# Performance work log

Measured on AMD Instinct MI355X. Metric: run time of the kernel, lower is better.

Reference implementation:

```python
import jax, jax.numpy as jnp
import numpy as np

K = 7          # local attention kernel size
PAD = 3        # (K-1)//2 so output spatial dims match input
GROUPS = 8

def unfold2d(x, k):
    # x: [B, C, H+k-1, W+k-1] -> patches [B, C, H, W, k*k] (kh-major, kw-minor, matching F.unfold)
    B, C, Hp, Wp = x.shape
    H, W = Hp - k + 1, Wp - k + 1
    return jnp.stack([x[:, :, i:i + H, j:j + W] for i in range(k) for j in range(k)], axis=-1)

def setup_inputs():
    key = jax.random.key(0)
    k1, k2, k3, k4, k5, k6 = jax.random.split(key, 6)
    B, Cin, H, W = 2, 256, 56, 56
    outc = 256
    scale = (2.0 / Cin) ** 0.5  # kaiming fan_out-ish init
    return {
        "feature_map": jax.random.normal(k1, (B, 2 * Cin, H, W), jnp.float32),
        "w_q": jax.random.normal(k2, (outc, Cin), jnp.float32) * scale,
        "w_k": jax.random.normal(k3, (outc, Cin), jnp.float32) * scale,
        "w_v": jax.random.normal(k4, (outc, Cin), jnp.float32) * scale,
        "rel_h": jax.random.normal(k5, (outc // 2, K), jnp.float32),
        "rel_w": jax.random.normal(k6, (outc // 2, K), jnp.float32),
    }

def reference(feature_map, w_q, w_k, w_v, rel_h, rel_w):
    B, C2, H, W = feature_map.shape
    Cin = C2 // 2
    fm_t0, fm_t1 = feature_map[:, :Cin], feature_map[:, Cin:]
    outc = w_q.shape[0]
    # 1x1 convs (bias=False)
    q = jnp.einsum('oc,bchw->bohw', w_q, fm_t1)                      # [B, outc, H, W]
    padded = jnp.pad(fm_t0, ((0, 0), (0, 0), (PAD, PAD), (PAD, PAD)))
    kk = jnp.einsum('oc,bchw->bohw', w_k, padded)
    vv = jnp.einsum('oc,bchw->bohw', w_v, padded)
    k_out = unfold2d(kk, K)                                          # [B, outc, H, W, K*K]
    v_out = unfold2d(vv, K)
    # relative position bias: first half channels get row bias, second half col bias
    half = outc // 2
    bias_h = jnp.broadcast_to(rel_h[:, :, None], (half, K, K)).reshape(half, K * K)
    bias_w = jnp.broadcast_to(rel_w[:, None, :], (half, K, K)).reshape(half, K * K)
    bias = jnp.concatenate([bias_h, bias_w], axis=0)                 # [outc, K*K]
    k_out = k_out + bias[None, :, None, None, :]
    G, Cg = GROUPS, outc // GROUPS
    qg = q.reshape(B, G, Cg, H, W)
    kg = k_out.reshape(B, G, Cg, H, W, K * K)
    vg = v_out.reshape(B, G, Cg, H, W, K * K)
    logits = jnp.einsum('bgchw,bgchwk->bghwk', qg, kg)
    wts = jax.nn.softmax(logits, axis=-1)
    out = jnp.einsum('bghwk,bgchwk->bgchw', wts, vg)
    return out.reshape(B, outc, H, W)
```

## Files before the change

### kernel.cpp

```cpp
#include <hip/hip_runtime.h>
#include <hip/hip_bf16.h>

#define B    2
#define CIN  256
#define H    56
#define W    56
#define OUTC 256
#define KS   7
#define PAD  3
#define G    8
#define CG   32
#define HP   62
#define WP   62
#define P1   (H * W)
#define P2   (HP * WP)

typedef __attribute__((ext_vector_type(2))) _Float16 h2;
typedef __attribute__((ext_vector_type(8))) _Float16 f16x8;
typedef __attribute__((ext_vector_type(8))) unsigned short ushort8;
typedef __attribute__((ext_vector_type(4))) float f32x4;

__device__ inline unsigned short f2h(float f) {
    const _Float16 h = (_Float16)f;
    return *(const unsigned short*)&h;
}

__device__ inline float fdot2(h2 a, h2 b, float c) {
#if defined(__has_builtin)
#if __has_builtin(__builtin_amdgcn_fdot2)
    return __builtin_amdgcn_fdot2(a, b, c, false);
#else
    return c + (float)a[0] * (float)b[0] + (float)a[1] * (float)b[1];
#endif
#else
    return c + (float)a[0] * (float)b[0] + (float)a[1] * (float)b[1];
#endif
}

__device__ inline float dot8(const f16x8 q, const f16x8 k, float s) {
    s = fdot2((h2){q[0], q[1]}, (h2){k[0], k[1]}, s);
    s = fdot2((h2){q[2], q[3]}, (h2){k[2], k[3]}, s);
    s = fdot2((h2){q[4], q[5]}, (h2){k[4], k[5]}, s);
    s = fdot2((h2){q[6], q[7]}, (h2){k[6], k[7]}, s);
    return s;
}

#define ASTR 40
__global__ __launch_bounds__(256, 2) void gemm_kernel(const float* __restrict__ fm,
                                                      const float* __restrict__ wq,
                                                      const float* __restrict__ wk,
                                                      const float* __restrict__ wv,
                                                      unsigned short* __restrict__ qi,
                                                      unsigned short* __restrict__ ki,
                                                      unsigned short* __restrict__ vi) {
    const int b = blockIdx.z;
    const bool isQ = blockIdx.y < 2;
    if (isQ && blockIdx.x >= 25) return;
    const int o0 = (isQ ? blockIdx.y : (blockIdx.y - 2)) * 128;
    const int n0 = blockIdx.x * 128;
    const int Nreal = isQ ? P1 : P2;
    const int Pstr  = isQ ? P1 : P2;

    const float* Wsrc;
    int orow0;
    if (isQ)            { Wsrc = wq; orow0 = o0; }
    else if (o0 < 256)  { Wsrc = wk; orow0 = o0; }
    else                { Wsrc = wv; orow0 = o0 - 256; }

    __shared__ unsigned short Alds[128 * ASTR];
    __shared__ unsigned short Blds[128 * ASTR];
    const int tid = threadIdx.x;
    const int lane = tid & 63;
    const int wave = tid >> 6;
    const int wr = (wave >> 1) * 64;
    const int wc = (wave & 1) * 64;
    const int lrow = lane & 15;
    const int quad = lane >> 4;

    const int arow = tid & 127;
    const int akc  = (tid >> 7) * 16;

    const int n = n0 + arow;
    int srcoff = -1;
    if (isQ) {
        if (n < P1) srcoff = n;
    } else {
        if (n < P2) {
            const int y = n / WP, x = n - y * WP;
            const int iy = y - PAD, ix = x - PAD;
            if (iy >= 0 && iy < H && ix >= 0 && ix < W) srcoff = iy * W + ix;
        }
    }
    const float* fmB = fm + ((size_t)b * (2 * CIN) + (isQ ? CIN : 0)) * P1;
    const float* wrow = Wsrc + (size_t)orow0 * CIN + (size_t)arow * CIN + akc;

    unsigned short* alp = Alds + arow * ASTR + akc;
    unsigned short* blp = Blds + arow * ASTR + akc;

    f32x4 acc[4][4] = {};

    float av[16], bv[16];
    {
        const float4 a0 = ((const float4*)wrow)[0];
        const float4 a1 = ((const float4*)wrow)[1];
        const float4 a2 = ((const float4*)wrow)[2];
        const float4 a3 = ((const float4*)wrow)[3];
        av[0]=a0.x; av[1]=a0.y; av[2]=a0.z; av[3]=a0.w;
        av[4]=a1.x; av[5]=a1.y; av[6]=a1.z; av[7]=a1.w;
        av[8]=a2.x; av[9]=a2.y; av[10]=a2.z; av[11]=a2.w;
        av[12]=a3.x; av[13]=a3.y; av[14]=a3.z; av[15]=a3.w;
        #pragma unroll
        for (int j = 0; j < 16; ++j)
            bv[j] = (srcoff >= 0) ? fmB[(size_t)(akc + j) * P1 + srcoff] : 0.f;
    }

    for (int kb = 0; kb < CIN / 32; ++kb) {
        {
            f16x8 p0, p1, p2, p3;
            #pragma unroll
            for (int j = 0; j < 8; ++j) {
                p0[j] = (_Float16)av[j];
                p1[j] = (_Float16)av[8 + j];
                p2[j] = (_Float16)bv[j];
                p3[j] = (_Float16)bv[8 + j];
            }
            *(f16x8*)(alp)     = p0;
            *(f16x8*)(alp + 8) = p1;
            *(f16x8*)(blp)     = p2;
            *(f16x8*)(blp + 8) = p3;
        }
        __syncthreads();
        if (kb < CIN / 32 - 1) {
            const int c0 = (kb + 1) * 32 + akc;
            const float* wnext = wrow + (kb + 1) * 32;
            const float4 a0 = ((const float4*)wnext)[0];
            const float4 a1 = ((const float4*)wnext)[1];
            const float4 a2 = ((const float4*)wnext)[2];
            const float4 a3 = ((const float4*)wnext)[3];
            av[0]=a0.x; av[1]=a0.y; av[2]=a0.z; av[3]=a0.w;
            av[4]=a1.x; av[5]=a1.y; av[6]=a1.z; av[7]=a1.w;
            av[8]=a2.x; av[9]=a2.y; av[10]=a2.z; av[11]=a2.w;
            av[12]=a3.x; av[13]=a3.y; av[14]=a3.z; av[15]=a3.w;
            #pragma unroll
            for (int j = 0; j < 16; ++j)
                bv[j] = (srcoff >= 0) ? fmB[(size_t)(c0 + j) * P1 + srcoff] : 0.f;
        }
        f16x8 af[4], bfr[4];
        #pragma unroll
        for (int mi = 0; mi < 4; ++mi)
            af[mi] = *(const f16x8*)&Alds[(wr + mi * 16 + lrow) * ASTR + quad * 8];
        #pragma unroll
        for (int ni = 0; ni < 4; ++ni)
            bfr[ni] = *(const f16x8*)&Blds[(wc + ni * 16 + lrow) * ASTR + quad * 8];
        #pragma unroll
        for (int mi = 0; mi < 4; ++mi)
            #pragma unroll
            for (int ni = 0; ni < 4; ++ni)
                acc[mi][ni] = __builtin_amdgcn_mfma_f32_16x16x32_f16(af[mi], bfr[ni], acc[mi][ni], 0, 0, 0);
        __syncthreads();
    }

    #pragma unroll
    for (int mi = 0; mi < 4; ++mi) {
        const int gmBase = o0 + wr + mi * 16 + quad * 4;
        int ch0;
        unsigned short* base;
        if (isQ)               { ch0 = gmBase;       base = qi; }
        else if (gmBase < 256) { ch0 = gmBase;       base = ki; }
        else                   { ch0 = gmBase - 256; base = vi; }
        const int g   = ch0 >> 5;
        const int sub = (ch0 >> 3) & 3;
        const int l8  = ch0 & 7;
        unsigned short* pbase = base + ((((size_t)b * 8 + g) * 4 + sub) * Pstr) * 8 + l8;
        #pragma unroll
        for (int ni = 0; ni < 4; ++ni) {
            const int gn = n0 + wc + ni * 16 + lrow;
            if (gn < Nreal) {
                ushort4 pk;
                pk.x = f2h(acc[mi][ni][0]);
                pk.y = f2h(acc[mi][ni][1]);
                pk.z = f2h(acc[mi][ni][2]);
                pk.w = f2h(acc[mi][ni][3]);
                *(ushort4*)(pbase + (size_t)gn * 8) = pk;
            }
        }
    }
}

#define NPOS4 620
#define HALFE 1240
__global__ __launch_bounds__(128) void attn_kernel(const unsigned short* __restrict__ qi,
                                                   const unsigned short* __restrict__ ki,
                                                   const unsigned short* __restrict__ vi,
                                                   const float* __restrict__ rel_h,
                                                   const float* __restrict__ rel_w,
                                                   float* __restrict__ out) {
    __shared__ f16x8 sbuf[2 * HALFE];

    const int b  = blockIdx.z;
    const int g  = blockIdx.y;
    const int r0 = blockIdx.x * 4;
    const int oc0 = g * CG;
    const int tid = threadIdx.x;
    const bool active = tid < 112;
    const int rp = tid / 56;
    const int cx = tid - rp * 56;
    const int pr0 = r0 + 2 * rp;
    const int pix0 = pr0 * W + cx;
    const int pix1 = pix0 + W;

    const size_t bg4 = ((size_t)b * 8 + g) * 4;
    const size_t rowoff8 = ((size_t)r0 * WP) * 8;

    f16x8* bufA = sbuf;
    f16x8* bufB = sbuf + HALFE;

    f16x8 qh0[4], qh1[4];
    if (active) {
        #pragma unroll
        for (int sub = 0; sub < 4; ++sub) {
            qh0[sub] = *(const f16x8*)(qi + ((bg4 + sub) * P1 + pix0) * 8);
            qh1[sub] = *(const f16x8*)(qi + ((bg4 + sub) * P1 + pix1) * 8);
        }
    }

    f16x8 st[10];
    {
        const unsigned short* gb = ki + bg4 * P2 * 8 + rowoff8;
        #pragma unroll
        for (int it = 0; it < 10; ++it) {
            const int e = tid + it * 128;
            if (e < HALFE) {
                const int sl = (e >= NPOS4);
                const int pos = e - (sl ? NPOS4 : 0);
                st[it] = *(const f16x8*)(gb + ((size_t)sl * P2 + pos) * 8);
            }
        }
        #pragma unroll
        for (int it = 0; it < 10; ++it) {
            const int e = tid + it * 128;
            if (e < HALFE) bufA[e] = st[it];
        }
    }
    __syncthreads();

    {
        const unsigned short* gb = ki + (bg4 + 2) * P2 * 8 + rowoff8;
        #pragma unroll
        for (int it = 0; it < 10; ++it) {
            const int e = tid + it * 128;
            if (e < HALFE) {
                const int sl = (e >= NPOS4);
                const int pos = e - (sl ? NPOS4 : 0);
                st[it] = *(const f16x8*)(gb + ((size_t)sl * P2 + pos) * 8);
            }
        }
    }

    float logits0[KS * KS], logits1[KS * KS];
    if (active) {
        const float* rel = (g < 4) ? (rel_h + oc0 * KS) : (rel_w + (oc0 - 128) * KS);
        float qf0[32], qf1[32];
        #pragma unroll
        for (int sub = 0; sub < 4; ++sub)
            #pragma unroll
            for (int j = 0; j < 8; ++j) {
                qf0[sub * 8 + j] = (float)qh0[sub][j];
                qf1[sub * 8 + j] = (float)qh1[sub][j];
            }
        float bd0[KS], bd1[KS];
        #pragma unroll
        for (int t = 0; t < KS; ++t) {
            float s0 = 0.f, s1 = 0.f;
            #pragma unroll
            for (int c = 0; c < 32; ++c) {
                const float r = rel[c * KS + t];
                s0 += qf0[c] * r;
                s1 += qf1[c] * r;
            }
            bd0[t] = s0; bd1[t] = s1;
        }
        #pragma unroll
        for (int i = 0; i < KS; ++i)
            #pragma unroll
            for (int j = 0; j < KS; ++j) {
                logits0[i * KS + j] = (g < 4) ? bd0[i] : bd0[j];
                logits1[i * KS + j] = (g < 4) ? bd1[i] : bd1[j];
            }

        #pragma unroll
        for (int s = 0; s < 2; ++s) {
            const f16x8 q0 = qh0[s];
            const f16x8 q1 = qh1[s];
            #pragma unroll
            for (int j = 0; j < KS; ++j) {
                #pragma unroll
                for (int ii = 0; ii < 8; ++ii) {
                    const f16x8 kv = bufA[s * NPOS4 + (2 * rp + ii) * WP + cx + j];
                    if (ii < 7)  logits0[ii * KS + j]       = dot8(q0, kv, logits0[ii * KS + j]);
                    if (ii >= 1) logits1[(ii - 1) * KS + j] = dot8(q1, kv, logits1[(ii - 1) * KS + j]);
                }
            }
        }
    }
    #pragma unroll
    for (int it = 0; it < 10; ++it) {
        const int e = tid + it * 128;
        if (e < HALFE) bufB[e] = st[it];
    }
    __syncthreads();

    {
        const unsigned short* gb = vi + bg4 * P2 * 8 + rowoff8;
        #pragma unroll
        for (int it = 0; it < 10; ++it) {
            const int e = tid + it * 128;
            if (e < HALFE) {
                const int sl = (e >= NPOS4);
                const int pos = e - (sl ? NPOS4 : 0);
                st[it] = *(const f16x8*)(gb + ((size_t)sl * P2 + pos) * 8);
            }
        }
    }

    if (active) {
        #pragma unroll
        for (int s = 0; s < 2; ++s) {
            const f16x8 q0 = qh0[2 + s];
            const f16x8 q1 = qh1[2 + s];
            #pragma unroll
            for (int j = 0; j < KS; ++j) {
                #pragma unroll
                for (int ii = 0; ii < 8; ++ii) {
                    const f16x8 kv = bufB[s * NPOS4 + (2 * rp + ii) * WP + cx + j];
                    if (ii < 7)  logits0[ii * KS + j]       = dot8(q0, kv, logits0[ii * KS + j]);
                    if (ii >= 1) logits1[(ii - 1) * KS + j] = dot8(q1, kv, logits1[(ii - 1) * KS + j]);
                }
            }
        }
        {
            float m = logits0[0];
            #pragma unroll
            for (int t = 1; t < KS * KS; ++t) m = fmaxf(m, logits0[t]);
            float sum = 0.f;
            #pragma unroll
            for (int t = 0; t < KS * KS; ++t) {
                const float e = __expf(logits0[t] - m);
                logits0[t] = e;
                sum += e;
            }
            const float inv = 1.f / sum;
            #pragma unroll
            for (int t = 0; t < KS * KS; ++t) logits0[t] *= inv;
        }
        {
            float m = logits1[0];
            #pragma unroll
            for (int t = 1; t < KS * KS; ++t) m = fmaxf(m, logits1[t]);
            float sum = 0.f;
            #pragma unroll
            for (int t = 0; t < KS * KS; ++t) {
                const float e = __expf(logits1[t] - m);
                logits1[t] = e;
                sum += e;
            }
            const float inv = 1.f / sum;
            #pragma unroll
            for (int t = 0; t < KS * KS; ++t) logits1[t] *= inv;
        }
    }
    #pragma unroll
    for (int it = 0; it < 10; ++it) {
        const int e = tid + it * 128;
        if (e < HALFE) bufA[e] = st[it];
    }
    __syncthreads();

    {
        const unsigned short* gb = vi + (bg4 + 2) * P2 * 8 + rowoff8;
        #pragma unroll
        for (int it = 0; it < 10; ++it) {
            const int e = tid + it * 128;
            if (e < HALFE) {
                const int sl = (e >= NPOS4);
                const int pos = e - (sl ? NPOS4 : 0);
                st[it] = *(const f16x8*)(gb + ((size_t)sl * P2 + pos) * 8);
            }
        }
    }

    if (active) {
        #pragma unroll
        for (int s = 0; s < 2; ++s) {
            float a0[8] = {}, a1[8] = {};
            #pragma unroll
            for (int j = 0; j < KS; ++j) {
                #pragma unroll
                for (int ii = 0; ii < 8; ++ii) {
                    const f16x8 v = bufA[s * NPOS4 + (2 * rp + ii) * WP + cx + j];
                    if (ii < 7) {
                        const float wt = logits0[ii * KS + j];
                        #pragma unroll
                        for (int c = 0; c < 8; ++c) a0[c] += wt * (float)v[c];
                    }
                    if (ii >= 1) {
                        const float wt = logits1[(ii - 1) * KS + j];
                        #pragma unroll
                        for (int c = 0; c < 8; ++c) a1[c] += wt * (float)v[c];
                    }
                }
            }
            float* op0 = out + ((size_t)b * OUTC + oc0 + s * 8) * P1 + pix0;
            float* op1 = out + ((size_t)b * OUTC + oc0 + s * 8) * P1 + pix1;
            #pragma unroll
            for (int c = 0; c < 8; ++c) {
                op0[(size_t)c * P1] = a0[c];
                op1[(size_t)c * P1] = a1[c];
            }
        }
    }
    #pragma unroll
    for (int it = 0; it < 10; ++it) {
        const int e = tid + it * 128;
        if (e < HALFE) bufB[e] = st[it];
    }
    __syncthreads();

    if (active) {
        #pragma unroll
        for (int s = 0; s < 2; ++s) {
            float a0[8] = {}, a1[8] = {};
            #pragma unroll
            for (int j = 0; j < KS; ++j) {
                #pragma unroll
                for (int ii = 0; ii < 8; ++ii) {
                    const f16x8 v = bufB[s * NPOS4 + (2 * rp + ii) * WP + cx + j];
                    if (ii < 7) {
                        const float wt = logits0[ii * KS + j];
                        #pragma unroll
                        for (int c = 0; c < 8; ++c) a0[c] += wt * (float)v[c];
                    }
                    if (ii >= 1) {
                        const float wt = logits1[(ii - 1) * KS + j];
                        #pragma unroll
                        for (int c = 0; c < 8; ++c) a1[c] += wt * (float)v[c];
                    }
                }
            }
            float* op0 = out + ((size_t)b * OUTC + oc0 + 16 + s * 8) * P1 + pix0;
            float* op1 = out + ((size_t)b * OUTC + oc0 + 16 + s * 8) * P1 + pix1;
            #pragma unroll
            for (int c = 0; c < 8; ++c) {
                op0[(size_t)c * P1] = a0[c];
                op1[(size_t)c * P1] = a1[c];
            }
        }
    }
}

extern "C" void kernel_launch(void* const* d_in, const int* in_sizes, int n_in,
                              void* d_out, int out_size, void* d_ws, size_t ws_size,
                              hipStream_t stream) {
    const float* fm = (const float*)d_in[0];
    const float* wq = (const float*)d_in[1];
    const float* wk = (const float*)d_in[2];
    const float* wv = (const float*)d_in[3];
    const float* rh = (const float*)d_in[4];
    const float* rw = (const float*)d_in[5];
    float* out = (float*)d_out;

    unsigned short* ws = (unsigned short*)d_ws;
    unsigned short* qi = ws;
    unsigned short* ki = qi + (size_t)B * OUTC * P1;
    unsigned short* vi = ki + (size_t)B * OUTC * P2;

    gemm_kernel<<<dim3(31, 6, B), 256, 0, stream>>>(fm, wq, wk, wv, qi, ki, vi);
    attn_kernel<<<dim3(H / 4, G, B), 128, 0, stream>>>(qi, ki, vi, rh, rw, out);
}
```

Baseline: 108.6 us.

## Replace LDS-staged attention with one-pixel-per-thread direct global loads

```diff
diff --git a/kernel.cpp b/kernel.cpp
--- a/kernel.cpp
+++ b/kernel.cpp
@@ -187,273 +187,103 @@
     }
 }
 
-#define NPOS4 620
-#define HALFE 1240
-__global__ __launch_bounds__(128) void attn_kernel(const unsigned short* __restrict__ qi,
+__global__ __launch_bounds__(256) void attn_kernel(const unsigned short* __restrict__ qi,
                                                    const unsigned short* __restrict__ ki,
                                                    const unsigned short* __restrict__ vi,
                                                    const float* __restrict__ rel_h,
                                                    const float* __restrict__ rel_w,
                                                    float* __restrict__ out) {
-    __shared__ f16x8 sbuf[2 * HALFE];
-
-    const int b  = blockIdx.z;
-    const int g  = blockIdx.y;
-    const int r0 = blockIdx.x * 4;
-    const int oc0 = g * CG;
+    const int b = blockIdx.z;
+    const int g = blockIdx.y;
     const int tid = threadIdx.x;
-    const bool active = tid < 112;
-    const int rp = tid / 56;
-    const int cx = tid - rp * 56;
-    const int pr0 = r0 + 2 * rp;
-    const int pix0 = pr0 * W + cx;
-    const int pix1 = pix0 + W;
-
-    const size_t bg4 = ((size_t)b * 8 + g) * 4;
-    const size_t rowoff8 = ((size_t)r0 * WP) * 8;
-
-    f16x8* bufA = sbuf;
-    f16x8* bufB = sbuf + HALFE;
-
-    f16x8 qh0[4], qh1[4];
-    if (active) {
-        #pragma unroll
-        for (int sub = 0; sub < 4; ++sub) {
-            qh0[sub] = *(const f16x8*)(qi + ((bg4 + sub) * P1 + pix0) * 8);
-            qh1[sub] = *(const f16x8*)(qi + ((bg4 + sub) * P1 + pix1) * 8);
-        }
-    }
-
-    f16x8 st[10];
+
+    int p = blockIdx.x * 256 + tid;
+    const bool act = p < P1;
+    if (!act) p = P1 - 1;
+
+    const int h = p / W;
+    const int w = p - h * W;
+    const int pos0 = h * WP + w;
+    const size_t bg4 = ((size_t)b * G + g) * 4;
+
+    f16x8 qh[4];
+    #pragma unroll
+    for (int s = 0; s < 4; ++s)
+        qh[s] = *(const f16x8*)(qi + ((bg4 + s) * P1 + p) * 8);
+
+    const float* rel = (g < 4) ? (rel_h + (size_t)g * CG * KS)
+                               : (rel_w + (size_t)(g - 4) * CG * KS);
+    float bd[KS];
+    #pragma unroll
+    for (int t = 0; t < KS; ++t) {
+        float s0 = 0.f;
+        #pragma unroll
+        for (int s = 0; s < 4; ++s)
+            #pragma unroll
+            for (int j = 0; j < 8; ++j)
+                s0 += (float)qh[s][j] * rel[(s * 8 + j) * KS + t];
+        bd[t] = s0;
+    }
+
+    float logits[KS * KS];
+    #pragma unroll
+    for (int i = 0; i < KS; ++i)
+        #pragma unroll
+        for (int j = 0; j < KS; ++j)
+            logits[i * KS + j] = (g < 4) ? bd[i] : bd[j];
+
+    #pragma unroll
+    for (int s = 0; s < 4; ++s) {
+        const unsigned short* kp = ki + ((bg4 + s) * P2 + pos0) * 8;
+        const f16x8 q = qh[s];
+        #pragma unroll
+        for (int i = 0; i < KS; ++i) {
+            const unsigned short* kr = kp + i * WP * 8;
+            #pragma unroll
+            for (int j = 0; j < KS; ++j) {
+                const f16x8 kv = *(const f16x8*)(kr + j * 8);
+                logits[i * KS + j] = dot8(q, kv, logits[i * KS + j]);
+            }
+        }
+    }
+
     {
-        const unsigned short* gb = ki + bg4 * P2 * 8 + rowoff8;
-        #pragma unroll
-        for (int it = 0; it < 10; ++it) {
-            const int e = tid + it * 128;
-            if (e < HALFE) {
-                const int sl = (e >= NPOS4);
-                const int pos = e - (sl ? NPOS4 : 0);
-                st[it] = *(const f16x8*)(gb + ((size_t)sl * P2 + pos) * 8);
+        float m = logits[0];
+        #pragma unroll
+        for (int t = 1; t < KS * KS; ++t) m = fmaxf(m, logits[t]);
+        float sum = 0.f;
+        #pragma unroll
+        for (int t = 0; t < KS * KS; ++t) {
+            const float e = __expf(logits[t] - m);
+            logits[t] = e;
+            sum += e;
+        }
+        const float inv = 1.f / sum;
+        #pragma unroll
+        for (int t = 0; t < KS * KS; ++t) logits[t] *= inv;
+    }
+
+    #pragma unroll
+    for (int s = 0; s < 4; ++s) {
+        const unsigned short* vp = vi + ((bg4 + s) * P2 + pos0) * 8;
+        float a[8] = {};
+        #pragma unroll
+        for (int i = 0; i < KS; ++i) {
+            const unsigned short* vr = vp + i * WP * 8;
+            #pragma unroll
+            for (int j = 0; j < KS; ++j) {
+                const f16x8 vv = *(const f16x8*)(vr + j * 8);
+                const float wt = logits[i * KS + j];
+                #pragma unroll
+                for (int c = 0; c < 8; ++c)
+                    a[c] += wt * (float)vv[c];
             }
         }
-        #pragma unroll
-        for (int it = 0; it < 10; ++it) {
-            const int e = tid + it * 128;
-            if (e < HALFE) bufA[e] = st[it];
-        }
-    }
-    __syncthreads();
-
-    {
-        const unsigned short* gb = ki + (bg4 + 2) * P2 * 8 + rowoff8;
-        #pragma unroll
-        for (int it = 0; it < 10; ++it) {
-            const int e = tid + it * 128;
-            if (e < HALFE) {
-                const int sl = (e >= NPOS4);
-                const int pos = e - (sl ? NPOS4 : 0);
-                st[it] = *(const f16x8*)(gb + ((size_t)sl * P2 + pos) * 8);
-            }
-        }
-    }
-
-    float logits0[KS * KS], logits1[KS * KS];
-    if (active) {
-        const float* rel = (g < 4) ? (rel_h + oc0 * KS) : (rel_w + (oc0 - 128) * KS);
-        float qf0[32], qf1[32];
-        #pragma unroll
-        for (int sub = 0; sub < 4; ++sub)
-            #pragma unroll
-            for (int j = 0; j < 8; ++j) {
-                qf0[sub * 8 + j] = (float)qh0[sub][j];
-                qf1[sub * 8 + j] = (float)qh1[sub][j];
-            }
-        float bd0[KS], bd1[KS];
-        #pragma unroll
-        for (int t = 0; t < KS; ++t) {
-            float s0 = 0.f, s1 = 0.f;
-            #pragma unroll
-            for (int c = 0; c < 32; ++c) {
-                const float r = rel[c * KS + t];
-                s0 += qf0[c] * r;
-                s1 += qf1[c] * r;
-            }
-            bd0[t] = s0; bd1[t] = s1;
-        }
-        #pragma unroll
-        for (int i = 0; i < KS; ++i)
-            #pragma unroll
-            for (int j = 0; j < KS; ++j) {
-                logits0[i * KS + j] = (g < 4) ? bd0[i] : bd0[j];
-                logits1[i * KS + j] = (g < 4) ? bd1[i] : bd1[j];
-            }
-
-        #pragma unroll
-        for (int s = 0; s < 2; ++s) {
-            const f16x8 q0 = qh0[s];
-            const f16x8 q1 = qh1[s];
-            #pragma unroll
-            for (int j = 0; j < KS; ++j) {
-                #pragma unroll
-                for (int ii = 0; ii < 8; ++ii) {
-                    const f16x8 kv = bufA[s * NPOS4 + (2 * rp + ii) * WP + cx + j];
-                    if (ii < 7)  logits0[ii * KS + j]       = dot8(q0, kv, logits0[ii * KS + j]);
-                    if (ii >= 1) logits1[(ii - 1) * KS + j] = dot8(q1, kv, logits1[(ii - 1) * KS + j]);
-                }
-            }
-        }
-    }
-    #pragma unroll
-    for (int it = 0; it < 10; ++it) {
-        const int e = tid + it * 128;
-        if (e < HALFE) bufB[e] = st[it];
-    }
-    __syncthreads();
-
-    {
-        const unsigned short* gb = vi + bg4 * P2 * 8 + rowoff8;
-        #pragma unroll
-        for (int it = 0; it < 10; ++it) {
-            const int e = tid + it * 128;
-            if (e < HALFE) {
-                const int sl = (e >= NPOS4);
-                const int pos = e - (sl ? NPOS4 : 0);
-                st[it] = *(const f16x8*)(gb + ((size_t)sl * P2 + pos) * 8);
-            }
-        }
-    }
-
-    if (active) {
-        #pragma unroll
-        for (int s = 0; s < 2; ++s) {
-            const f16x8 q0 = qh0[2 + s];
-            const f16x8 q1 = qh1[2 + s];
-            #pragma unroll
-            for (int j = 0; j < KS; ++j) {
-                #pragma unroll
-                for (int ii = 0; ii < 8; ++ii) {
-                    const f16x8 kv = bufB[s * NPOS4 + (2 * rp + ii) * WP + cx + j];
-                    if (ii < 7)  logits0[ii * KS + j]       = dot8(q0, kv, logits0[ii * KS + j]);
-                    if (ii >= 1) logits1[(ii - 1) * KS + j] = dot8(q1, kv, logits1[(ii - 1) * KS + j]);
-                }
-            }
-        }
-        {
-            float m = logits0[0];
-            #pragma unroll
-            for (int t = 1; t < KS * KS; ++t) m = fmaxf(m, logits0[t]);
-            float sum = 0.f;
-            #pragma unroll
-            for (int t = 0; t < KS * KS; ++t) {
-                const float e = __expf(logits0[t] - m);
-                logits0[t] = e;
-                sum += e;
-            }
-            const float inv = 1.f / sum;
-            #pragma unroll
-            for (int t = 0; t < KS * KS; ++t) logits0[t] *= inv;
-        }
-        {
-            float m = logits1[0];
-            #pragma unroll
-            for (int t = 1; t < KS * KS; ++t) m = fmaxf(m, logits1[t]);
-            float sum = 0.f;
-            #pragma unroll
-            for (int t = 0; t < KS * KS; ++t) {
-                const float e = __expf(logits1[t] - m);
-                logits1[t] = e;
-                sum += e;
-            }
-            const float inv = 1.f / sum;
-            #pragma unroll
-            for (int t = 0; t < KS * KS; ++t) logits1[t] *= inv;
-        }
-    }
-    #pragma unroll
-    for (int it = 0; it < 10; ++it) {
-        const int e = tid + it * 128;
-        if (e < HALFE) bufA[e] = st[it];
-    }
-    __syncthreads();
-
-    {
-        const unsigned short* gb = vi + (bg4 + 2) * P2 * 8 + rowoff8;
-        #pragma unroll
-        for (int it = 0; it < 10; ++it) {
-            const int e = tid + it * 128;
-            if (e < HALFE) {
-                const int sl = (e >= NPOS4);
-                const int pos = e - (sl ? NPOS4 : 0);
-                st[it] = *(const f16x8*)(gb + ((size_t)sl * P2 + pos) * 8);
-            }
-        }
-    }
-
-    if (active) {
-        #pragma unroll
-        for (int s = 0; s < 2; ++s) {
-            float a0[8] = {}, a1[8] = {};
-            #pragma unroll
-            for (int j = 0; j < KS; ++j) {
-                #pragma unroll
-                for (int ii = 0; ii < 8; ++ii) {
-                    const f16x8 v = bufA[s * NPOS4 + (2 * rp + ii) * WP + cx + j];
-                    if (ii < 7) {
-                        const float wt = logits0[ii * KS + j];
-                        #pragma unroll
-                        for (int c = 0; c < 8; ++c) a0[c] += wt * (float)v[c];
-                    }
-                    if (ii >= 1) {
-                        const float wt = logits1[(ii - 1) * KS + j];
-                        #pragma unroll
-                        for (int c = 0; c < 8; ++c) a1[c] += wt * (float)v[c];
-                    }
-                }
-            }
-            float* op0 = out + ((size_t)b * OUTC + oc0 + s * 8) * P1 + pix0;
-            float* op1 = out + ((size_t)b * OUTC + oc0 + s * 8) * P1 + pix1;
-            #pragma unroll
-            for (int c = 0; c < 8; ++c) {
-                op0[(size_t)c * P1] = a0[c];
-                op1[(size_t)c * P1] = a1[c];
-            }
-        }
-    }
-    #pragma unroll
-    for (int it = 0; it < 10; ++it) {
-        const int e = tid + it * 128;
-        if (e < HALFE) bufB[e] = st[it];
-    }
-    __syncthreads();
-
-    if (active) {
-        #pragma unroll
-        for (int s = 0; s < 2; ++s) {
-            float a0[8] = {}, a1[8] = {};
-            #pragma unroll
-            for (int j = 0; j < KS; ++j) {
-                #pragma unroll
-                for (int ii = 0; ii < 8; ++ii) {
-                    const f16x8 v = bufB[s * NPOS4 + (2 * rp + ii) * WP + cx + j];
-                    if (ii < 7) {
-                        const float wt = logits0[ii * KS + j];
-                        #pragma unroll
-                        for (int c = 0; c < 8; ++c) a0[c] += wt * (float)v[c];
-                    }
-                    if (ii >= 1) {
-                        const float wt = logits1[(ii - 1) * KS + j];
-                        #pragma unroll
-                        for (int c = 0; c < 8; ++c) a1[c] += wt * (float)v[c];
-                    }
-                }
-            }
-            float* op0 = out + ((size_t)b * OUTC + oc0 + 16 + s * 8) * P1 + pix0;
-            float* op1 = out + ((size_t)b * OUTC + oc0 + 16 + s * 8) * P1 + pix1;
-            #pragma unroll
-            for (int c = 0; c < 8; ++c) {
-                op0[(size_t)c * P1] = a0[c];
-                op1[(size_t)c * P1] = a1[c];
-            }
+        if (act) {
+            float* op = out + ((size_t)b * OUTC + g * CG + s * 8) * P1 + p;
+            #pragma unroll
+            for (int c = 0; c < 8; ++c)
+                op[(size_t)c * P1] = a[c];
         }
     }
 }
@@ -475,5 +305,5 @@
     unsigned short* vi = ki + (size_t)B * OUTC * P2;
 
     gemm_kernel<<<dim3(31, 6, B), 256, 0, stream>>>(fm, wq, wk, wv, qi, ki, vi);
-    attn_kernel<<<dim3(H / 4, G, B), 128, 0, stream>>>(qi, ki, vi, rh, rw, out);
-}
+    attn_kernel<<<dim3((P1 + 255) / 256, G, B), 256, 0, stream>>>(qi, ki, vi, rh, rw, out);
+}
```

Result: slower. 114.3 us (+5.2%).
